# Kernel tuning notes

Hardware: AMD Instinct MI355X
Metric: run time of the kernel (lower is better)

Reference implementation:

```python
import jax, jax.numpy as jnp
import numpy as np

NEG_SLOPE = 0.2


def setup_inputs() -> dict:
    key = jax.random.key(0)
    k1, k2, k3, k4, k5 = jax.random.split(key, 5)
    N, D, E = 10000, 128, 640000
    feat = jax.random.normal(k1, (N, D), dtype=jnp.float32)
    # nn.Linear weight [out_feats, in_feats]; scale like default init
    fc_weight = jax.random.normal(k2, (D, D), dtype=jnp.float32) / jnp.sqrt(jnp.float32(D))
    attn = jax.random.normal(k3, (1, 1, D), dtype=jnp.float32) * 0.1
    eps = jnp.zeros((1,), dtype=jnp.float32)
    src = jax.random.randint(k4, (E,), 0, N, dtype=jnp.int32)
    dst = jax.random.randint(k5, (E,), 0, N, dtype=jnp.int32)
    return {"feat": feat, "fc_weight": fc_weight, "attn": attn, "eps": eps,
            "src": src, "dst": dst}


def reference(feat, fc_weight, attn, eps, src, dst):
    N = feat.shape[0]
    # --- get_attention_tensor (attn_type='MX', num_heads=1) ---
    proj = feat @ fc_weight.T                      # [N, out]
    el = proj[src]                                  # [E, out] u side
    er = proj[dst]                                  # [E, out] v side
    a = attn.reshape(-1)                            # [out]
    e = jnp.sum(jax.nn.leaky_relu(el + er, NEG_SLOPE) * a, axis=-1)   # [E]
    gate = jax.nn.sigmoid(jnp.sum(el * er, axis=-1))                  # [E] sigmoid(u_dot_v)
    w = jax.nn.sigmoid(e * gate)                    # [E] final per-edge weight
    # --- message passing: u_mul_e('h','_edge_weight') with 'mean' reduce ---
    msg = feat[src] * w[:, None]                    # [E, D]
    neigh_sum = jax.ops.segment_sum(msg, dst, num_segments=N)         # [N, D]
    deg = jax.ops.segment_sum(jnp.ones_like(w), dst, num_segments=N)  # [N]
    neigh = neigh_sum / jnp.maximum(deg, 1.0)[:, None]                # mean; 0 for deg-0
    # --- node update ---
    rst = (1.0 + eps[0]) * feat + neigh
    return rst
```

## Files before the change

kernel.cpp:

```cpp
#include <hip/hip_runtime.h>

#define DD 128
#define CAP 128
#define BH 128

typedef unsigned short ushort_t;
typedef __attribute__((ext_vector_type(8))) short bf16x8;
typedef __attribute__((ext_vector_type(4))) float f32x4;

__device__ __forceinline__ unsigned short f2bf(float f) {
    unsigned u = __float_as_uint(f);
    u = (u + 0x7FFFu + ((u >> 16) & 1u)) >> 16;
    return (unsigned short)u;
}
__device__ __forceinline__ float bflo(unsigned v) { return __uint_as_float(v << 16); }
__device__ __forceinline__ float bfhi(unsigned v) { return __uint_as_float(v & 0xFFFF0000u); }
__device__ __forceinline__ unsigned pack2(float a, float b) {
    return (unsigned)f2bf(a) | ((unsigned)f2bf(b) << 16);
}
__device__ __forceinline__ bf16x8 cvt8(const float* __restrict__ p) {
    float4 f0 = *(const float4*)p;
    float4 f1 = *(const float4*)(p + 4);
    bf16x8 v;
    v[0] = (short)f2bf(f0.x); v[1] = (short)f2bf(f0.y);
    v[2] = (short)f2bf(f0.z); v[3] = (short)f2bf(f0.w);
    v[4] = (short)f2bf(f1.x); v[5] = (short)f2bf(f1.y);
    v[6] = (short)f2bf(f1.z); v[7] = (short)f2bf(f1.w);
    return v;
}

__global__ __launch_bounds__(256) void k1_hist_gemm(
    const float* __restrict__ feat, const float* __restrict__ W,
    const float* __restrict__ attn, const int* __restrict__ dst,
    ushort_t* __restrict__ projb, float* __restrict__ dotA,
    ushort_t* __restrict__ cnt, int N, int E, int CE)
{
    extern __shared__ unsigned h[];
    int b = (int)blockIdx.x;
    if (b < BH) {
        int NW = (N + 1) >> 1;
        for (int i = threadIdx.x; i < NW; i += 256) h[i] = 0;
        __syncthreads();
        int base = b * CE;
        for (int k = threadIdx.x; k < CE; k += 256) {
            int i = base + k;
            if (i < E) {
                int d = dst[i];
                atomicAdd(&h[d >> 1], (d & 1) ? 0x10000u : 1u);
            }
        }
        __syncthreads();
        ushort_t* crow = cnt + (size_t)b * N;
        for (int i = threadIdx.x; i < N; i += 256)
            crow[i] = (ushort_t)((h[i >> 1] >> ((i & 1) * 16)) & 0xFFFFu);
        return;
    }
    int rowTile = (b - BH) * 4 + ((int)threadIdx.x >> 6);
    if (rowTile * 16 >= N) return;
    int lane = threadIdx.x & 63;
    int m = lane & 15;
    int quad = lane >> 4;
    const float* arow = feat + (size_t)(rowTile * 16 + m) * DD + quad * 8;
    bf16x8 afr[4];
#pragma unroll
    for (int ks = 0; ks < 4; ++ks) afr[ks] = cvt8(arow + ks * 32);
    float dacc0 = 0.f, dacc1 = 0.f, dacc2 = 0.f, dacc3 = 0.f;
#pragma unroll
    for (int ct = 0; ct < 8; ++ct) {
        const float* brow = W + (size_t)(ct * 16 + m) * DD + quad * 8;
        f32x4 acc = {0.f, 0.f, 0.f, 0.f};
#pragma unroll
        for (int ks = 0; ks < 4; ++ks) {
            bf16x8 bb = cvt8(brow + ks * 32);
            acc = __builtin_amdgcn_mfma_f32_16x16x32_bf16(afr[ks], bb, acc, 0, 0, 0);
        }
        ushort_t* orow = projb + (size_t)(rowTile * 16 + quad * 4) * DD
                       + ct * 16 + m;
#pragma unroll
        for (int r = 0; r < 4; ++r)
            orow[(size_t)r * DD] = f2bf(acc[r]);
        float av = 0.6f * attn[ct * 16 + m];
        dacc0 = fmaf(av, acc[0], dacc0);
        dacc1 = fmaf(av, acc[1], dacc1);
        dacc2 = fmaf(av, acc[2], dacc2);
        dacc3 = fmaf(av, acc[3], dacc3);
    }
#pragma unroll
    for (int o = 1; o < 16; o <<= 1) {
        dacc0 += __shfl_xor(dacc0, o); dacc1 += __shfl_xor(dacc1, o);
        dacc2 += __shfl_xor(dacc2, o); dacc3 += __shfl_xor(dacc3, o);
    }
    if (m == 0) {
        int rbase = rowTile * 16 + quad * 4;
        if (rbase + 3 < N) {
            dotA[rbase]     = dacc0;
            dotA[rbase + 1] = dacc1;
            dotA[rbase + 2] = dacc2;
            dotA[rbase + 3] = dacc3;
        }
    }
}

__global__ __launch_bounds__(256) void k2_scan_cast(
    const float* __restrict__ feat, const ushort_t* __restrict__ cnt,
    ushort_t* __restrict__ offs, int* __restrict__ totals,
    ushort_t* __restrict__ featb, int N, int SC)
{
    int b = (int)blockIdx.x;
    if (b < SC) {
        int bin = b * 256 + (int)threadIdx.x;
        if (bin >= N) return;
        int run = 0;
#pragma unroll 8
        for (int blk = 0; blk < BH; ++blk) {
            int v = cnt[(size_t)blk * N + bin];
            offs[(size_t)blk * N + bin] = (ushort_t)run;
            run += v;
        }
        totals[bin] = run;
        return;
    }
    size_t total = (size_t)N * DD;
    size_t idx = ((size_t)(b - SC) * 256 + threadIdx.x) * 8;
    if (idx + 7 < total) {
        float4 f0 = *(const float4*)(feat + idx);
        float4 f1 = *(const float4*)(feat + idx + 4);
        uint4 o;
        o.x = pack2(f0.x, f0.y); o.y = pack2(f0.z, f0.w);
        o.z = pack2(f1.x, f1.y); o.w = pack2(f1.z, f1.w);
        *(uint4*)(featb + idx) = o;
    } else {
        for (size_t i = idx; i < total; ++i) featb[i] = f2bf(feat[i]);
    }
}

__global__ __launch_bounds__(256) void k3_scatter(
    const int* __restrict__ src, const int* __restrict__ dst,
    const ushort_t* __restrict__ offs, ushort_t* __restrict__ sorted,
    int N, int E, int CE)
{
    extern __shared__ unsigned h[];
    int b = (int)blockIdx.x;
    int NW = (N + 1) >> 1;
    for (int i = threadIdx.x; i < NW; i += 256) h[i] = 0;
    __syncthreads();
    const ushort_t* orow = offs + (size_t)b * N;
    int base = b * CE;
    for (int k = (int)threadIdx.x * 4; k < CE; k += 1024) {
        int i = base + k;
        if (i + 3 < E && k + 3 < CE) {
            int4 s4 = *(const int4*)(src + i);
            int4 d4 = *(const int4*)(dst + i);
            unsigned r0 = atomicAdd(&h[d4.x >> 1], (d4.x & 1) ? 0x10000u : 1u);
            unsigned r1 = atomicAdd(&h[d4.y >> 1], (d4.y & 1) ? 0x10000u : 1u);
            unsigned r2 = atomicAdd(&h[d4.z >> 1], (d4.z & 1) ? 0x10000u : 1u);
            unsigned r3 = atomicAdd(&h[d4.w >> 1], (d4.w & 1) ? 0x10000u : 1u);
            unsigned p0 = (unsigned)orow[d4.x] + ((r0 >> ((d4.x & 1) * 16)) & 0xFFFFu);
            unsigned p1 = (unsigned)orow[d4.y] + ((r1 >> ((d4.y & 1) * 16)) & 0xFFFFu);
            unsigned p2 = (unsigned)orow[d4.z] + ((r2 >> ((d4.z & 1) * 16)) & 0xFFFFu);
            unsigned p3 = (unsigned)orow[d4.w] + ((r3 >> ((d4.w & 1) * 16)) & 0xFFFFu);
            if (p0 < CAP) sorted[(size_t)d4.x * CAP + p0] = (ushort_t)s4.x;
            if (p1 < CAP) sorted[(size_t)d4.y * CAP + p1] = (ushort_t)s4.y;
            if (p2 < CAP) sorted[(size_t)d4.z * CAP + p2] = (ushort_t)s4.z;
            if (p3 < CAP) sorted[(size_t)d4.w * CAP + p3] = (ushort_t)s4.w;
        } else {
            for (int q = 0; q < 4 && k + q < CE; ++q) {
                int ii = base + k + q;
                if (ii < E) {
                    int d = dst[ii];
                    unsigned r = atomicAdd(&h[d >> 1], (d & 1) ? 0x10000u : 1u);
                    unsigned pos = (unsigned)orow[d]
                                 + ((r >> ((d & 1) * 16)) & 0xFFFFu);
                    if (pos < CAP) sorted[(size_t)d * CAP + pos] = (ushort_t)src[ii];
                }
            }
        }
    }
}

__global__ __launch_bounds__(256) void seg_agg(
    const ushort_t* __restrict__ projb, const ushort_t* __restrict__ featb,
    const float* __restrict__ feat, const float* __restrict__ attn,
    const float* __restrict__ dotA, const ushort_t* __restrict__ sorted,
    const int* __restrict__ totals, const float* __restrict__ eps,
    float* __restrict__ out, int N)
{
    int wid = (int)((blockIdx.x * (size_t)blockDim.x + threadIdx.x) >> 6);
    if (wid >= N) return;
    int lane = threadIdx.x & 63;
    int g   = lane >> 3;
    int sub = lane & 7;

    const uint4* projv = (const uint4*)projb;
    const uint4* featv = (const uint4*)featb;

    int m = min(totals[wid], CAP);
    const ushort_t* lst = sorted + (size_t)wid * CAP;

    uint4 ev0 = projv[(size_t)wid * 16 + 2 * sub];
    uint4 ev1 = projv[(size_t)wid * 16 + 2 * sub + 1];
    float er[16] = {
        bflo(ev0.x), bfhi(ev0.x), bflo(ev0.y), bfhi(ev0.y),
        bflo(ev0.z), bfhi(ev0.z), bflo(ev0.w), bfhi(ev0.w),
        bflo(ev1.x), bfhi(ev1.x), bflo(ev1.y), bfhi(ev1.y),
        bflo(ev1.z), bfhi(ev1.z), bflo(ev1.w), bfhi(ev1.w)};
    float av[16];
#pragma unroll
    for (int k = 0; k < 16; ++k) av[k] = 0.4f * attn[16 * sub + k];
    float dAr = dotA[wid];
    float c[16];
#pragma unroll
    for (int k = 0; k < 16; ++k) c[k] = 0.f;

    uint4 apv0, apv1, afv0, afv1; float adAl = 0.f;
    uint4 bpv0, bpv1, bfv0, bfv1; float bdAl = 0.f;

    auto ldst = [&](int idx, uint4& pv0, uint4& pv1, uint4& fv0, uint4& fv1,
                    float& dAl) {
        int s = (idx < m) ? (int)lst[idx] : 0;
        pv0 = projv[(size_t)s * 16 + 2 * sub];
        pv1 = projv[(size_t)s * 16 + 2 * sub + 1];
        fv0 = featv[(size_t)s * 16 + 2 * sub];
        fv1 = featv[(size_t)s * 16 + 2 * sub + 1];
        dAl = dotA[s];
    };

    int i = g;
    if (i < m)     ldst(i,     apv0, apv1, afv0, afv1, adAl);
    if (i + 8 < m) ldst(i + 8, bpv0, bpv1, bfv0, bfv1, bdAl);

    while (i < m) {
        uint4 cpv0, cpv1, cfv0, cfv1; float cdAl;
        ldst(i + 16, cpv0, cpv1, cfv0, cfv1, cdAl);
        float el[16] = {
            bflo(apv0.x), bfhi(apv0.x), bflo(apv0.y), bfhi(apv0.y),
            bflo(apv0.z), bfhi(apv0.z), bflo(apv0.w), bfhi(apv0.w),
            bflo(apv1.x), bfhi(apv1.x), bflo(apv1.y), bfhi(apv1.y),
            bflo(apv1.z), bfhi(apv1.z), bflo(apv1.w), bfhi(apv1.w)};
        float gp = 0.f, ad = 0.f;
#pragma unroll
        for (int k = 0; k < 16; ++k) {
            gp = fmaf(el[k], er[k], gp);
            ad = fmaf(fabsf(el[k] + er[k]), av[k], ad);
        }
#pragma unroll
        for (int o = 1; o <= 4; o <<= 1) {
            gp += __shfl_xor(gp, o);
            ad += __shfl_xor(ad, o);
        }
        float ep = adAl + dAr + ad;
        float gate = 1.f / (1.f + __expf(-gp));
        float w = 1.f / (1.f + __expf(-ep * gate));
        float fl[16] = {
            bflo(afv0.x), bfhi(afv0.x), bflo(afv0.y), bfhi(afv0.y),
            bflo(afv0.z), bfhi(afv0.z), bflo(afv0.w), bfhi(afv0.w),
            bflo(afv1.x), bfhi(afv1.x), bflo(afv1.y), bfhi(afv1.y),
            bflo(afv1.z), bfhi(afv1.z), bflo(afv1.w), bfhi(afv1.w)};
#pragma unroll
        for (int k = 0; k < 16; ++k) c[k] = fmaf(fl[k], w, c[k]);
        apv0 = bpv0; apv1 = bpv1; afv0 = bfv0; afv1 = bfv1; adAl = bdAl;
        bpv0 = cpv0; bpv1 = cpv1; bfv0 = cfv0; bfv1 = cfv1; bdAl = cdAl;
        i += 8;
    }
#pragma unroll
    for (int o = 8; o <= 32; o <<= 1) {
#pragma unroll
        for (int k = 0; k < 16; ++k) c[k] += __shfl_xor(c[k], o);
    }
    if (g == 0) {
        float inv = 1.f / fmaxf((float)m, 1.f);
        float sc = 1.f + eps[0];
        const f32x4* fsrc = (const f32x4*)feat + (size_t)wid * 32 + 4 * sub;
        f32x4* od = (f32x4*)out + (size_t)wid * 32 + 4 * sub;
#pragma unroll
        for (int q = 0; q < 4; ++q) {
            f32x4 f = __builtin_nontemporal_load(&fsrc[q]);
            f32x4 o;
            o[0] = fmaf(sc, f[0], c[4 * q] * inv);
            o[1] = fmaf(sc, f[1], c[4 * q + 1] * inv);
            o[2] = fmaf(sc, f[2], c[4 * q + 2] * inv);
            o[3] = fmaf(sc, f[3], c[4 * q + 3] * inv);
            __builtin_nontemporal_store(o, &od[q]);
        }
    }
}

extern "C" void kernel_launch(void* const* d_in, const int* in_sizes, int n_in,
                              void* d_out, int out_size, void* d_ws, size_t ws_size,
                              hipStream_t stream) {
    const float* feat = (const float*)d_in[0];
    const float* W    = (const float*)d_in[1];
    const float* attn = (const float*)d_in[2];
    const float* eps  = (const float*)d_in[3];
    const int*   src  = (const int*)d_in[4];
    const int*   dst  = (const int*)d_in[5];
    int N = in_sizes[0] / DD;
    int E = in_sizes[4];

    ushort_t* projb  = (ushort_t*)d_ws;
    ushort_t* featb  = projb + (size_t)N * DD;
    ushort_t* sorted = featb + (size_t)N * DD;
    ushort_t* cnt    = sorted + (size_t)N * CAP;
    ushort_t* offs   = cnt + (size_t)BH * N;
    int*      totals = (int*)(offs + (size_t)BH * N);
    float*    dotA   = (float*)(totals + N);

    int CE = (E + BH - 1) / BH;
    int GB = ((N + 15) / 16 + 3) / 4;
    int SC = (N + 255) / 256;
    int CB = (N * DD + 2047) / 2048;
    size_t ldsB = (size_t)((N + 1) / 2) * sizeof(unsigned);

    k1_hist_gemm<<<BH + GB, 256, ldsB, stream>>>(
        feat, W, attn, dst, projb, dotA, cnt, N, E, CE);
    k2_scan_cast<<<SC + CB, 256, 0, stream>>>(
        feat, cnt, offs, totals, featb, N, SC);
    k3_scatter<<<BH, 256, ldsB, stream>>>(src, dst, offs, sorted, N, E, CE);
    seg_agg<<<(N * 64 + 255) / 256, 256, 0, stream>>>(
        projb, featb, feat, attn, dotA, sorted, totals, eps,
        (float*)d_out, N);
}
```

Before: 138.1 us.

## Fuse all four stages into one persistent cooperative kernel with grid syncs

Merges the histogram+GEMM, scan+cast, scatter, and segment aggregation kernels into a single persistent cooperative kernel that loops over virtual blocks and separates the phases with grid.sync(). The aim is to remove the launch overhead and inter-kernel gaps of four launches. In exchange it adds grid-wide barriers and limits parallelism to a capped persistent grid. The per-node aggregation, previously one wave per node, now runs as a grid-stride loop. Each block also carries the 20KB LDS allocation in every phase, which may reduce occupancy.

```diff
diff --git a/kernel.cpp b/kernel.cpp
--- a/kernel.cpp
+++ b/kernel.cpp
@@ -1,4 +1,7 @@
 #include <hip/hip_runtime.h>
+#include <hip/hip_cooperative_groups.h>
+
+namespace cg = cooperative_groups;
 
 #define DD 128
 #define CAP 128
@@ -29,258 +32,249 @@
     return v;
 }
 
-__global__ __launch_bounds__(256) void k1_hist_gemm(
+__global__ __launch_bounds__(256, 4) void fused_all(
     const float* __restrict__ feat, const float* __restrict__ W,
-    const float* __restrict__ attn, const int* __restrict__ dst,
-    ushort_t* __restrict__ projb, float* __restrict__ dotA,
-    ushort_t* __restrict__ cnt, int N, int E, int CE)
+    const float* __restrict__ attn, const int* __restrict__ src,
+    const int* __restrict__ dst, const float* __restrict__ eps,
+    ushort_t* __restrict__ featb, ushort_t* __restrict__ projb,
+    float* __restrict__ dotA, ushort_t* __restrict__ cnt,
+    ushort_t* __restrict__ offs, int* __restrict__ totals,
+    ushort_t* __restrict__ sorted, float* __restrict__ out,
+    int N, int E, int CE, int GB, int CB, int SC)
 {
+    cg::grid_group grid = cg::this_grid();
     extern __shared__ unsigned h[];
-    int b = (int)blockIdx.x;
-    if (b < BH) {
-        int NW = (N + 1) >> 1;
+    int NW = (N + 1) >> 1;
+    int G = (int)gridDim.x;
+
+    for (int vb = (int)blockIdx.x; vb < BH + GB + CB; vb += G) {
+        if (vb < BH) {
+            for (int i = threadIdx.x; i < NW; i += 256) h[i] = 0;
+            __syncthreads();
+            int base = vb * CE;
+            for (int k = threadIdx.x; k < CE; k += 256) {
+                int i = base + k;
+                if (i < E) {
+                    int d = dst[i];
+                    atomicAdd(&h[d >> 1], (d & 1) ? 0x10000u : 1u);
+                }
+            }
+            __syncthreads();
+            ushort_t* crow = cnt + (size_t)vb * N;
+            for (int i = threadIdx.x; i < N; i += 256)
+                crow[i] = (ushort_t)((h[i >> 1] >> ((i & 1) * 16)) & 0xFFFFu);
+            __syncthreads();
+        } else if (vb < BH + GB) {
+            int rowTile = (vb - BH) * 4 + ((int)threadIdx.x >> 6);
+            if (rowTile * 16 < N) {
+                int lane = threadIdx.x & 63;
+                int m = lane & 15;
+                int quad = lane >> 4;
+                const float* arow = feat + (size_t)(rowTile * 16 + m) * DD + quad * 8;
+                bf16x8 afr[4];
+#pragma unroll
+                for (int ks = 0; ks < 4; ++ks) afr[ks] = cvt8(arow + ks * 32);
+                float dacc0 = 0.f, dacc1 = 0.f, dacc2 = 0.f, dacc3 = 0.f;
+#pragma unroll
+                for (int ct = 0; ct < 8; ++ct) {
+                    const float* brow = W + (size_t)(ct * 16 + m) * DD + quad * 8;
+                    f32x4 acc = {0.f, 0.f, 0.f, 0.f};
+#pragma unroll
+                    for (int ks = 0; ks < 4; ++ks) {
+                        bf16x8 bb = cvt8(brow + ks * 32);
+                        acc = __builtin_amdgcn_mfma_f32_16x16x32_bf16(
+                            afr[ks], bb, acc, 0, 0, 0);
+                    }
+                    ushort_t* orow = projb
+                        + (size_t)(rowTile * 16 + quad * 4) * DD + ct * 16 + m;
+#pragma unroll
+                    for (int r = 0; r < 4; ++r)
+                        orow[(size_t)r * DD] = f2bf(acc[r]);
+                    float av = 0.6f * attn[ct * 16 + m];
+                    dacc0 = fmaf(av, acc[0], dacc0);
+                    dacc1 = fmaf(av, acc[1], dacc1);
+                    dacc2 = fmaf(av, acc[2], dacc2);
+                    dacc3 = fmaf(av, acc[3], dacc3);
+                }
+#pragma unroll
+                for (int o = 1; o < 16; o <<= 1) {
+                    dacc0 += __shfl_xor(dacc0, o); dacc1 += __shfl_xor(dacc1, o);
+                    dacc2 += __shfl_xor(dacc2, o); dacc3 += __shfl_xor(dacc3, o);
+                }
+                if (m == 0) {
+                    int rbase = rowTile * 16 + quad * 4;
+                    if (rbase + 3 < N) {
+                        dotA[rbase]     = dacc0;
+                        dotA[rbase + 1] = dacc1;
+                        dotA[rbase + 2] = dacc2;
+                        dotA[rbase + 3] = dacc3;
+                    }
+                }
+            }
+        } else {
+            size_t total = (size_t)N * DD;
+            size_t idx = ((size_t)(vb - BH - GB) * 256 + threadIdx.x) * 8;
+            if (idx + 7 < total) {
+                float4 f0 = *(const float4*)(feat + idx);
+                float4 f1 = *(const float4*)(feat + idx + 4);
+                uint4 o;
+                o.x = pack2(f0.x, f0.y); o.y = pack2(f0.z, f0.w);
+                o.z = pack2(f1.x, f1.y); o.w = pack2(f1.z, f1.w);
+                *(uint4*)(featb + idx) = o;
+            } else {
+                for (size_t i = idx; i < total; ++i) featb[i] = f2bf(feat[i]);
+            }
+        }
+    }
+    grid.sync();
+
+    if ((int)blockIdx.x < SC) {
+        int bin = (int)blockIdx.x * 256 + (int)threadIdx.x;
+        if (bin < N) {
+            int run = 0;
+#pragma unroll 8
+            for (int blk = 0; blk < BH; ++blk) {
+                int v = cnt[(size_t)blk * N + bin];
+                offs[(size_t)blk * N + bin] = (ushort_t)run;
+                run += v;
+            }
+            totals[bin] = run;
+        }
+    }
+    grid.sync();
+
+    for (int vb = (int)blockIdx.x; vb < BH; vb += G) {
         for (int i = threadIdx.x; i < NW; i += 256) h[i] = 0;
         __syncthreads();
-        int base = b * CE;
-        for (int k = threadIdx.x; k < CE; k += 256) {
+        const ushort_t* orow = offs + (size_t)vb * N;
+        int base = vb * CE;
+        for (int k = (int)threadIdx.x * 4; k < CE; k += 1024) {
             int i = base + k;
-            if (i < E) {
-                int d = dst[i];
-                atomicAdd(&h[d >> 1], (d & 1) ? 0x10000u : 1u);
+            if (i + 3 < E && k + 3 < CE) {
+                int4 s4 = *(const int4*)(src + i);
+                int4 d4 = *(const int4*)(dst + i);
+                unsigned r0 = atomicAdd(&h[d4.x >> 1], (d4.x & 1) ? 0x10000u : 1u);
+                unsigned r1 = atomicAdd(&h[d4.y >> 1], (d4.y & 1) ? 0x10000u : 1u);
+                unsigned r2 = atomicAdd(&h[d4.z >> 1], (d4.z & 1) ? 0x10000u : 1u);
+                unsigned r3 = atomicAdd(&h[d4.w >> 1], (d4.w & 1) ? 0x10000u : 1u);
+                unsigned p0 = (unsigned)orow[d4.x] + ((r0 >> ((d4.x & 1) * 16)) & 0xFFFFu);
+                unsigned p1 = (unsigned)orow[d4.y] + ((r1 >> ((d4.y & 1) * 16)) & 0xFFFFu);
+                unsigned p2 = (unsigned)orow[d4.z] + ((r2 >> ((d4.z & 1) * 16)) & 0xFFFFu);
+                unsigned p3 = (unsigned)orow[d4.w] + ((r3 >> ((d4.w & 1) * 16)) & 0xFFFFu);
+                if (p0 < CAP) sorted[(size_t)d4.x * CAP + p0] = (ushort_t)s4.x;
+                if (p1 < CAP) sorted[(size_t)d4.y * CAP + p1] = (ushort_t)s4.y;
+                if (p2 < CAP) sorted[(size_t)d4.z * CAP + p2] = (ushort_t)s4.z;
+                if (p3 < CAP) sorted[(size_t)d4.w * CAP + p3] = (ushort_t)s4.w;
+            } else {
+                for (int q = 0; q < 4 && k + q < CE; ++q) {
+                    int ii = base + k + q;
+                    if (ii < E) {
+                        int d = dst[ii];
+                        unsigned r = atomicAdd(&h[d >> 1], (d & 1) ? 0x10000u : 1u);
+                        unsigned pos = (unsigned)orow[d]
+                                     + ((r >> ((d & 1) * 16)) & 0xFFFFu);
+                        if (pos < CAP) sorted[(size_t)d * CAP + pos] = (ushort_t)src[ii];
+                    }
+                }
             }
         }
         __syncthreads();
-        ushort_t* crow = cnt + (size_t)b * N;
-        for (int i = threadIdx.x; i < N; i += 256)
-            crow[i] = (ushort_t)((h[i >> 1] >> ((i & 1) * 16)) & 0xFFFFu);
-        return;
     }
-    int rowTile = (b - BH) * 4 + ((int)threadIdx.x >> 6);
-    if (rowTile * 16 >= N) return;
-    int lane = threadIdx.x & 63;
-    int m = lane & 15;
-    int quad = lane >> 4;
-    const float* arow = feat + (size_t)(rowTile * 16 + m) * DD + quad * 8;
-    bf16x8 afr[4];
-#pragma unroll
-    for (int ks = 0; ks < 4; ++ks) afr[ks] = cvt8(arow + ks * 32);
-    float dacc0 = 0.f, dacc1 = 0.f, dacc2 = 0.f, dacc3 = 0.f;
-#pragma unroll
-    for (int ct = 0; ct < 8; ++ct) {
-        const float* brow = W + (size_t)(ct * 16 + m) * DD + quad * 8;
-        f32x4 acc = {0.f, 0.f, 0.f, 0.f};
-#pragma unroll
-        for (int ks = 0; ks < 4; ++ks) {
-            bf16x8 bb = cvt8(brow + ks * 32);
-            acc = __builtin_amdgcn_mfma_f32_16x16x32_bf16(afr[ks], bb, acc, 0, 0, 0);
-        }
-        ushort_t* orow = projb + (size_t)(rowTile * 16 + quad * 4) * DD
-                       + ct * 16 + m;
-#pragma unroll
-        for (int r = 0; r < 4; ++r)
-            orow[(size_t)r * DD] = f2bf(acc[r]);
-        float av = 0.6f * attn[ct * 16 + m];
-        dacc0 = fmaf(av, acc[0], dacc0);
-        dacc1 = fmaf(av, acc[1], dacc1);
-        dacc2 = fmaf(av, acc[2], dacc2);
-        dacc3 = fmaf(av, acc[3], dacc3);
-    }
-#pragma unroll
-    for (int o = 1; o < 16; o <<= 1) {
-        dacc0 += __shfl_xor(dacc0, o); dacc1 += __shfl_xor(dacc1, o);
-        dacc2 += __shfl_xor(dacc2, o); dacc3 += __shfl_xor(dacc3, o);
-    }
-    if (m == 0) {
-        int rbase = rowTile * 16 + quad * 4;
-        if (rbase + 3 < N) {
-            dotA[rbase]     = dacc0;
-            dotA[rbase + 1] = dacc1;
-            dotA[rbase + 2] = dacc2;
-            dotA[rbase + 3] = dacc3;
-        }
-    }
-}
-
-__global__ __launch_bounds__(256) void k2_scan_cast(
-    const float* __restrict__ feat, const ushort_t* __restrict__ cnt,
-    ushort_t* __restrict__ offs, int* __restrict__ totals,
-    ushort_t* __restrict__ featb, int N, int SC)
-{
-    int b = (int)blockIdx.x;
-    if (b < SC) {
-        int bin = b * 256 + (int)threadIdx.x;
-        if (bin >= N) return;
-        int run = 0;
-#pragma unroll 8
-        for (int blk = 0; blk < BH; ++blk) {
-            int v = cnt[(size_t)blk * N + bin];
-            offs[(size_t)blk * N + bin] = (ushort_t)run;
-            run += v;
-        }
-        totals[bin] = run;
-        return;
-    }
-    size_t total = (size_t)N * DD;
-    size_t idx = ((size_t)(b - SC) * 256 + threadIdx.x) * 8;
-    if (idx + 7 < total) {
-        float4 f0 = *(const float4*)(feat + idx);
-        float4 f1 = *(const float4*)(feat + idx + 4);
-        uint4 o;
-        o.x = pack2(f0.x, f0.y); o.y = pack2(f0.z, f0.w);
-        o.z = pack2(f1.x, f1.y); o.w = pack2(f1.z, f1.w);
-        *(uint4*)(featb + idx) = o;
-    } else {
-        for (size_t i = idx; i < total; ++i) featb[i] = f2bf(feat[i]);
-    }
-}
-
-__global__ __launch_bounds__(256) void k3_scatter(
-    const int* __restrict__ src, const int* __restrict__ dst,
-    const ushort_t* __restrict__ offs, ushort_t* __restrict__ sorted,
-    int N, int E, int CE)
-{
-    extern __shared__ unsigned h[];
-    int b = (int)blockIdx.x;
-    int NW = (N + 1) >> 1;
-    for (int i = threadIdx.x; i < NW; i += 256) h[i] = 0;
-    __syncthreads();
-    const ushort_t* orow = offs + (size_t)b * N;
-    int base = b * CE;
-    for (int k = (int)threadIdx.x * 4; k < CE; k += 1024) {
-        int i = base + k;
-        if (i + 3 < E && k + 3 < CE) {
-            int4 s4 = *(const int4*)(src + i);
-            int4 d4 = *(const int4*)(dst + i);
-            unsigned r0 = atomicAdd(&h[d4.x >> 1], (d4.x & 1) ? 0x10000u : 1u);
-            unsigned r1 = atomicAdd(&h[d4.y >> 1], (d4.y & 1) ? 0x10000u : 1u);
-            unsigned r2 = atomicAdd(&h[d4.z >> 1], (d4.z & 1) ? 0x10000u : 1u);
-            unsigned r3 = atomicAdd(&h[d4.w >> 1], (d4.w & 1) ? 0x10000u : 1u);
-            unsigned p0 = (unsigned)orow[d4.x] + ((r0 >> ((d4.x & 1) * 16)) & 0xFFFFu);
-            unsigned p1 = (unsigned)orow[d4.y] + ((r1 >> ((d4.y & 1) * 16)) & 0xFFFFu);
-            unsigned p2 = (unsigned)orow[d4.z] + ((r2 >> ((d4.z & 1) * 16)) & 0xFFFFu);
-            unsigned p3 = (unsigned)orow[d4.w] + ((r3 >> ((d4.w & 1) * 16)) & 0xFFFFu);
-            if (p0 < CAP) sorted[(size_t)d4.x * CAP + p0] = (ushort_t)s4.x;
-            if (p1 < CAP) sorted[(size_t)d4.y * CAP + p1] = (ushort_t)s4.y;
-            if (p2 < CAP) sorted[(size_t)d4.z * CAP + p2] = (ushort_t)s4.z;
-            if (p3 < CAP) sorted[(size_t)d4.w * CAP + p3] = (ushort_t)s4.w;
-        } else {
-            for (int q = 0; q < 4 && k + q < CE; ++q) {
-                int ii = base + k + q;
-                if (ii < E) {
-                    int d = dst[ii];
-                    unsigned r = atomicAdd(&h[d >> 1], (d & 1) ? 0x10000u : 1u);
-                    unsigned pos = (unsigned)orow[d]
-                                 + ((r >> ((d & 1) * 16)) & 0xFFFFu);
-                    if (pos < CAP) sorted[(size_t)d * CAP + pos] = (ushort_t)src[ii];
-                }
-            }
-        }
-    }
-}
-
-__global__ __launch_bounds__(256) void seg_agg(
-    const ushort_t* __restrict__ projb, const ushort_t* __restrict__ featb,
-    const float* __restrict__ feat, const float* __restrict__ attn,
-    const float* __restrict__ dotA, const ushort_t* __restrict__ sorted,
-    const int* __restrict__ totals, const float* __restrict__ eps,
-    float* __restrict__ out, int N)
-{
-    int wid = (int)((blockIdx.x * (size_t)blockDim.x + threadIdx.x) >> 6);
-    if (wid >= N) return;
+    grid.sync();
+
     int lane = threadIdx.x & 63;
     int g   = lane >> 3;
     int sub = lane & 7;
-
     const uint4* projv = (const uint4*)projb;
     const uint4* featv = (const uint4*)featb;
-
-    int m = min(totals[wid], CAP);
-    const ushort_t* lst = sorted + (size_t)wid * CAP;
-
-    uint4 ev0 = projv[(size_t)wid * 16 + 2 * sub];
-    uint4 ev1 = projv[(size_t)wid * 16 + 2 * sub + 1];
-    float er[16] = {
-        bflo(ev0.x), bfhi(ev0.x), bflo(ev0.y), bfhi(ev0.y),
-        bflo(ev0.z), bfhi(ev0.z), bflo(ev0.w), bfhi(ev0.w),
-        bflo(ev1.x), bfhi(ev1.x), bflo(ev1.y), bfhi(ev1.y),
-        bflo(ev1.z), bfhi(ev1.z), bflo(ev1.w), bfhi(ev1.w)};
     float av[16];
 #pragma unroll
     for (int k = 0; k < 16; ++k) av[k] = 0.4f * attn[16 * sub + k];
-    float dAr = dotA[wid];
-    float c[16];
-#pragma unroll
-    for (int k = 0; k < 16; ++k) c[k] = 0.f;
-
-    uint4 apv0, apv1, afv0, afv1; float adAl = 0.f;
-    uint4 bpv0, bpv1, bfv0, bfv1; float bdAl = 0.f;
-
-    auto ldst = [&](int idx, uint4& pv0, uint4& pv1, uint4& fv0, uint4& fv1,
-                    float& dAl) {
-        int s = (idx < m) ? (int)lst[idx] : 0;
-        pv0 = projv[(size_t)s * 16 + 2 * sub];
-        pv1 = projv[(size_t)s * 16 + 2 * sub + 1];
-        fv0 = featv[(size_t)s * 16 + 2 * sub];
-        fv1 = featv[(size_t)s * 16 + 2 * sub + 1];
-        dAl = dotA[s];
-    };
-
-    int i = g;
-    if (i < m)     ldst(i,     apv0, apv1, afv0, afv1, adAl);
-    if (i + 8 < m) ldst(i + 8, bpv0, bpv1, bfv0, bfv1, bdAl);
-
-    while (i < m) {
-        uint4 cpv0, cpv1, cfv0, cfv1; float cdAl;
-        ldst(i + 16, cpv0, cpv1, cfv0, cfv1, cdAl);
-        float el[16] = {
-            bflo(apv0.x), bfhi(apv0.x), bflo(apv0.y), bfhi(apv0.y),
-            bflo(apv0.z), bfhi(apv0.z), bflo(apv0.w), bfhi(apv0.w),
-            bflo(apv1.x), bfhi(apv1.x), bflo(apv1.y), bfhi(apv1.y),
-            bflo(apv1.z), bfhi(apv1.z), bflo(apv1.w), bfhi(apv1.w)};
-        float gp = 0.f, ad = 0.f;
-#pragma unroll
-        for (int k = 0; k < 16; ++k) {
-            gp = fmaf(el[k], er[k], gp);
-            ad = fmaf(fabsf(el[k] + er[k]), av[k], ad);
-        }
-#pragma unroll
-        for (int o = 1; o <= 4; o <<= 1) {
-            gp += __shfl_xor(gp, o);
-            ad += __shfl_xor(ad, o);
-        }
-        float ep = adAl + dAr + ad;
-        float gate = 1.f / (1.f + __expf(-gp));
-        float w = 1.f / (1.f + __expf(-ep * gate));
-        float fl[16] = {
-            bflo(afv0.x), bfhi(afv0.x), bflo(afv0.y), bfhi(afv0.y),
-            bflo(afv0.z), bfhi(afv0.z), bflo(afv0.w), bfhi(afv0.w),
-            bflo(afv1.x), bfhi(afv1.x), bflo(afv1.y), bfhi(afv1.y),
-            bflo(afv1.z), bfhi(afv1.z), bflo(afv1.w), bfhi(afv1.w)};
-#pragma unroll
-        for (int k = 0; k < 16; ++k) c[k] = fmaf(fl[k], w, c[k]);
-        apv0 = bpv0; apv1 = bpv1; afv0 = bfv0; afv1 = bfv1; adAl = bdAl;
-        bpv0 = cpv0; bpv1 = cpv1; bfv0 = cfv0; bfv1 = cfv1; bdAl = cdAl;
-        i += 8;
-    }
-#pragma unroll
-    for (int o = 8; o <= 32; o <<= 1) {
-#pragma unroll
-        for (int k = 0; k < 16; ++k) c[k] += __shfl_xor(c[k], o);
-    }
-    if (g == 0) {
-        float inv = 1.f / fmaxf((float)m, 1.f);
-        float sc = 1.f + eps[0];
-        const f32x4* fsrc = (const f32x4*)feat + (size_t)wid * 32 + 4 * sub;
-        f32x4* od = (f32x4*)out + (size_t)wid * 32 + 4 * sub;
-#pragma unroll
-        for (int q = 0; q < 4; ++q) {
-            f32x4 f = __builtin_nontemporal_load(&fsrc[q]);
-            f32x4 o;
-            o[0] = fmaf(sc, f[0], c[4 * q] * inv);
-            o[1] = fmaf(sc, f[1], c[4 * q + 1] * inv);
-            o[2] = fmaf(sc, f[2], c[4 * q + 2] * inv);
-            o[3] = fmaf(sc, f[3], c[4 * q + 3] * inv);
-            __builtin_nontemporal_store(o, &od[q]);
+    float sc = 1.f + eps[0];
+    int totalWaves = G * 4;
+    int gw = (int)blockIdx.x * 4 + ((int)threadIdx.x >> 6);
+
+    for (int wid = gw; wid < N; wid += totalWaves) {
+        int m = min(totals[wid], CAP);
+        const ushort_t* lst = sorted + (size_t)wid * CAP;
+        uint4 ev0 = projv[(size_t)wid * 16 + 2 * sub];
+        uint4 ev1 = projv[(size_t)wid * 16 + 2 * sub + 1];
+        float er[16] = {
+            bflo(ev0.x), bfhi(ev0.x), bflo(ev0.y), bfhi(ev0.y),
+            bflo(ev0.z), bfhi(ev0.z), bflo(ev0.w), bfhi(ev0.w),
+            bflo(ev1.x), bfhi(ev1.x), bflo(ev1.y), bfhi(ev1.y),
+            bflo(ev1.z), bfhi(ev1.z), bflo(ev1.w), bfhi(ev1.w)};
+        float dAr = dotA[wid];
+        float c[16];
+#pragma unroll
+        for (int k = 0; k < 16; ++k) c[k] = 0.f;
+
+        uint4 apv0, apv1, afv0, afv1; float adAl = 0.f;
+        uint4 bpv0, bpv1, bfv0, bfv1; float bdAl = 0.f;
+        auto ldst = [&](int idx, uint4& pv0, uint4& pv1, uint4& fv0,
+                        uint4& fv1, float& dAl) {
+            int s = (idx < m) ? (int)lst[idx] : 0;
+            pv0 = projv[(size_t)s * 16 + 2 * sub];
+            pv1 = projv[(size_t)s * 16 + 2 * sub + 1];
+            fv0 = featv[(size_t)s * 16 + 2 * sub];
+            fv1 = featv[(size_t)s * 16 + 2 * sub + 1];
+            dAl = dotA[s];
+        };
+        int i = g;
+        if (i < m)     ldst(i,     apv0, apv1, afv0, afv1, adAl);
+        if (i + 8 < m) ldst(i + 8, bpv0, bpv1, bfv0, bfv1, bdAl);
+        while (i < m) {
+            uint4 cpv0, cpv1, cfv0, cfv1; float cdAl;
+            ldst(i + 16, cpv0, cpv1, cfv0, cfv1, cdAl);
+            float el[16] = {
+                bflo(apv0.x), bfhi(apv0.x), bflo(apv0.y), bfhi(apv0.y),
+                bflo(apv0.z), bfhi(apv0.z), bflo(apv0.w), bfhi(apv0.w),
+                bflo(apv1.x), bfhi(apv1.x), bflo(apv1.y), bfhi(apv1.y),
+                bflo(apv1.z), bfhi(apv1.z), bflo(apv1.w), bfhi(apv1.w)};
+            float gp = 0.f, ad = 0.f;
+#pragma unroll
+            for (int k = 0; k < 16; ++k) {
+                gp = fmaf(el[k], er[k], gp);
+                ad = fmaf(fabsf(el[k] + er[k]), av[k], ad);
+            }
+#pragma unroll
+            for (int o = 1; o <= 4; o <<= 1) {
+                gp += __shfl_xor(gp, o);
+                ad += __shfl_xor(ad, o);
+            }
+            float ep = adAl + dAr + ad;
+            float gate = 1.f / (1.f + __expf(-gp));
+            float w = 1.f / (1.f + __expf(-ep * gate));
+            float fl[16] = {
+                bflo(afv0.x), bfhi(afv0.x), bflo(afv0.y), bfhi(afv0.y),
+                bflo(afv0.z), bfhi(afv0.z), bflo(afv0.w), bfhi(afv0.w),
+                bflo(afv1.x), bfhi(afv1.x), bflo(afv1.y), bfhi(afv1.y),
+                bflo(afv1.z), bfhi(afv1.z), bflo(afv1.w), bfhi(afv1.w)};
+#pragma unroll
+            for (int k = 0; k < 16; ++k) c[k] = fmaf(fl[k], w, c[k]);
+            apv0 = bpv0; apv1 = bpv1; afv0 = bfv0; afv1 = bfv1; adAl = bdAl;
+            bpv0 = cpv0; bpv1 = cpv1; bfv0 = cfv0; bfv1 = cfv1; bdAl = cdAl;
+            i += 8;
+        }
+#pragma unroll
+        for (int o = 8; o <= 32; o <<= 1) {
+#pragma unroll
+            for (int k = 0; k < 16; ++k) c[k] += __shfl_xor(c[k], o);
+        }
+        if (g == 0) {
+            float inv = 1.f / fmaxf((float)m, 1.f);
+            const f32x4* fsrc = (const f32x4*)feat + (size_t)wid * 32 + 4 * sub;
+            f32x4* od = (f32x4*)out + (size_t)wid * 32 + 4 * sub;
+#pragma unroll
+            for (int q = 0; q < 4; ++q) {
+                f32x4 f = __builtin_nontemporal_load(&fsrc[q]);
+                f32x4 o;
+                o[0] = fmaf(sc, f[0], c[4 * q] * inv);
+                o[1] = fmaf(sc, f[1], c[4 * q + 1] * inv);
+                o[2] = fmaf(sc, f[2], c[4 * q + 2] * inv);
+                o[3] = fmaf(sc, f[3], c[4 * q + 3] * inv);
+                __builtin_nontemporal_store(o, &od[q]);
+            }
         }
     }
 }
@@ -304,19 +298,27 @@
     ushort_t* offs   = cnt + (size_t)BH * N;
     int*      totals = (int*)(offs + (size_t)BH * N);
     float*    dotA   = (float*)(totals + N);
+    float*    out    = (float*)d_out;
 
     int CE = (E + BH - 1) / BH;
     int GB = ((N + 15) / 16 + 3) / 4;
+    int CB = (N * DD + 2047) / 2048;
     int SC = (N + 255) / 256;
-    int CB = (N * DD + 2047) / 2048;
     size_t ldsB = (size_t)((N + 1) / 2) * sizeof(unsigned);
 
-    k1_hist_gemm<<<BH + GB, 256, ldsB, stream>>>(
-        feat, W, attn, dst, projb, dotA, cnt, N, E, CE);
-    k2_scan_cast<<<SC + CB, 256, 0, stream>>>(
-        feat, cnt, offs, totals, featb, N, SC);
-    k3_scatter<<<BH, 256, ldsB, stream>>>(src, dst, offs, sorted, N, E, CE);
-    seg_agg<<<(N * 64 + 255) / 256, 256, 0, stream>>>(
-        projb, featb, feat, attn, dotA, sorted, totals, eps,
-        (float*)d_out, N);
-}
+    int maxBlocksPerCU = 0;
+    hipOccupancyMaxActiveBlocksPerMultiprocessor(
+        &maxBlocksPerCU, (const void*)fused_all, 256, ldsB);
+    int G = maxBlocksPerCU * 256;
+    if (G > 1024) G = 1024;
+    if (G < 256) G = 256;
+
+    void* args[] = {
+        (void*)&feat, (void*)&W, (void*)&attn, (void*)&src, (void*)&dst,
+        (void*)&eps, (void*)&featb, (void*)&projb, (void*)&dotA,
+        (void*)&cnt, (void*)&offs, (void*)&totals, (void*)&sorted,
+        (void*)&out, (void*)&N, (void*)&E, (void*)&CE, (void*)&GB,
+        (void*)&CB, (void*)&SC};
+    hipLaunchCooperativeKernel((const void*)fused_all, dim3(G), dim3(256),
+                               args, (unsigned)ldsB, stream);
+}
```

After: 337.6 us. 145% more time.

## Merge cast into GEMM kernel and fuse scan with scatter via flag

Applied to the files above, without the earlier changes.

Moves the feature-to-bf16 cast into the histogram/GEMM launch, and merges the per-bin prefix scan with the scatter kernel. Scatter blocks spin on a global atomic counter until every scan block has released its offsets. This removes one kernel launch and its inter-kernel gap. It relies on the scan blocks being scheduled before or alongside the spinning scatter blocks; with SC+BH blocks this should fit on the device, but the spin-wait can stall or deadlock if residency assumptions fail.

```diff
diff --git a/kernel.cpp b/kernel.cpp
--- a/kernel.cpp
+++ b/kernel.cpp
@@ -29,14 +29,16 @@
     return v;
 }
 
-__global__ __launch_bounds__(256) void k1_hist_gemm(
+__global__ __launch_bounds__(256) void k1_hist_gemm_cast(
     const float* __restrict__ feat, const float* __restrict__ W,
     const float* __restrict__ attn, const int* __restrict__ dst,
-    ushort_t* __restrict__ projb, float* __restrict__ dotA,
-    ushort_t* __restrict__ cnt, int N, int E, int CE)
+    ushort_t* __restrict__ featb, ushort_t* __restrict__ projb,
+    float* __restrict__ dotA, ushort_t* __restrict__ cnt,
+    int* __restrict__ flag, int N, int E, int GB, int CE)
 {
     extern __shared__ unsigned h[];
     int b = (int)blockIdx.x;
+    if (b == BH && threadIdx.x == 0) *flag = 0;
     if (b < BH) {
         int NW = (N + 1) >> 1;
         for (int i = threadIdx.x; i < NW; i += 256) h[i] = 0;
@@ -55,73 +57,55 @@
             crow[i] = (ushort_t)((h[i >> 1] >> ((i & 1) * 16)) & 0xFFFFu);
         return;
     }
-    int rowTile = (b - BH) * 4 + ((int)threadIdx.x >> 6);
-    if (rowTile * 16 >= N) return;
-    int lane = threadIdx.x & 63;
-    int m = lane & 15;
-    int quad = lane >> 4;
-    const float* arow = feat + (size_t)(rowTile * 16 + m) * DD + quad * 8;
-    bf16x8 afr[4];
-#pragma unroll
-    for (int ks = 0; ks < 4; ++ks) afr[ks] = cvt8(arow + ks * 32);
-    float dacc0 = 0.f, dacc1 = 0.f, dacc2 = 0.f, dacc3 = 0.f;
-#pragma unroll
-    for (int ct = 0; ct < 8; ++ct) {
-        const float* brow = W + (size_t)(ct * 16 + m) * DD + quad * 8;
-        f32x4 acc = {0.f, 0.f, 0.f, 0.f};
-#pragma unroll
-        for (int ks = 0; ks < 4; ++ks) {
-            bf16x8 bb = cvt8(brow + ks * 32);
-            acc = __builtin_amdgcn_mfma_f32_16x16x32_bf16(afr[ks], bb, acc, 0, 0, 0);
-        }
-        ushort_t* orow = projb + (size_t)(rowTile * 16 + quad * 4) * DD
-                       + ct * 16 + m;
-#pragma unroll
-        for (int r = 0; r < 4; ++r)
-            orow[(size_t)r * DD] = f2bf(acc[r]);
-        float av = 0.6f * attn[ct * 16 + m];
-        dacc0 = fmaf(av, acc[0], dacc0);
-        dacc1 = fmaf(av, acc[1], dacc1);
-        dacc2 = fmaf(av, acc[2], dacc2);
-        dacc3 = fmaf(av, acc[3], dacc3);
-    }
-#pragma unroll
-    for (int o = 1; o < 16; o <<= 1) {
-        dacc0 += __shfl_xor(dacc0, o); dacc1 += __shfl_xor(dacc1, o);
-        dacc2 += __shfl_xor(dacc2, o); dacc3 += __shfl_xor(dacc3, o);
-    }
-    if (m == 0) {
-        int rbase = rowTile * 16 + quad * 4;
-        if (rbase + 3 < N) {
-            dotA[rbase]     = dacc0;
-            dotA[rbase + 1] = dacc1;
-            dotA[rbase + 2] = dacc2;
-            dotA[rbase + 3] = dacc3;
-        }
-    }
-}
-
-__global__ __launch_bounds__(256) void k2_scan_cast(
-    const float* __restrict__ feat, const ushort_t* __restrict__ cnt,
-    ushort_t* __restrict__ offs, int* __restrict__ totals,
-    ushort_t* __restrict__ featb, int N, int SC)
-{
-    int b = (int)blockIdx.x;
-    if (b < SC) {
-        int bin = b * 256 + (int)threadIdx.x;
-        if (bin >= N) return;
-        int run = 0;
-#pragma unroll 8
-        for (int blk = 0; blk < BH; ++blk) {
-            int v = cnt[(size_t)blk * N + bin];
-            offs[(size_t)blk * N + bin] = (ushort_t)run;
-            run += v;
-        }
-        totals[bin] = run;
+    if (b < BH + GB) {
+        int rowTile = (b - BH) * 4 + ((int)threadIdx.x >> 6);
+        if (rowTile * 16 >= N) return;
+        int lane = threadIdx.x & 63;
+        int m = lane & 15;
+        int quad = lane >> 4;
+        const float* arow = feat + (size_t)(rowTile * 16 + m) * DD + quad * 8;
+        bf16x8 afr[4];
+#pragma unroll
+        for (int ks = 0; ks < 4; ++ks) afr[ks] = cvt8(arow + ks * 32);
+        float dacc0 = 0.f, dacc1 = 0.f, dacc2 = 0.f, dacc3 = 0.f;
+#pragma unroll
+        for (int ct = 0; ct < 8; ++ct) {
+            const float* brow = W + (size_t)(ct * 16 + m) * DD + quad * 8;
+            f32x4 acc = {0.f, 0.f, 0.f, 0.f};
+#pragma unroll
+            for (int ks = 0; ks < 4; ++ks) {
+                bf16x8 bb = cvt8(brow + ks * 32);
+                acc = __builtin_amdgcn_mfma_f32_16x16x32_bf16(afr[ks], bb, acc, 0, 0, 0);
+            }
+            ushort_t* orow = projb + (size_t)(rowTile * 16 + quad * 4) * DD
+                           + ct * 16 + m;
+#pragma unroll
+            for (int r = 0; r < 4; ++r)
+                orow[(size_t)r * DD] = f2bf(acc[r]);
+            float av = 0.6f * attn[ct * 16 + m];
+            dacc0 = fmaf(av, acc[0], dacc0);
+            dacc1 = fmaf(av, acc[1], dacc1);
+            dacc2 = fmaf(av, acc[2], dacc2);
+            dacc3 = fmaf(av, acc[3], dacc3);
+        }
+#pragma unroll
+        for (int o = 1; o < 16; o <<= 1) {
+            dacc0 += __shfl_xor(dacc0, o); dacc1 += __shfl_xor(dacc1, o);
+            dacc2 += __shfl_xor(dacc2, o); dacc3 += __shfl_xor(dacc3, o);
+        }
+        if (m == 0) {
+            int rbase = rowTile * 16 + quad * 4;
+            if (rbase + 3 < N) {
+                dotA[rbase]     = dacc0;
+                dotA[rbase + 1] = dacc1;
+                dotA[rbase + 2] = dacc2;
+                dotA[rbase + 3] = dacc3;
+            }
+        }
         return;
     }
     size_t total = (size_t)N * DD;
-    size_t idx = ((size_t)(b - SC) * 256 + threadIdx.x) * 8;
+    size_t idx = ((size_t)(b - BH - GB) * 256 + threadIdx.x) * 8;
     if (idx + 7 < total) {
         float4 f0 = *(const float4*)(feat + idx);
         float4 f1 = *(const float4*)(feat + idx + 4);
@@ -134,18 +118,46 @@
     }
 }
 
-__global__ __launch_bounds__(256) void k3_scatter(
+__global__ __launch_bounds__(256) void k23_scan_scatter(
     const int* __restrict__ src, const int* __restrict__ dst,
-    const ushort_t* __restrict__ offs, ushort_t* __restrict__ sorted,
-    int N, int E, int CE)
+    const ushort_t* __restrict__ cnt, ushort_t* __restrict__ offs,
+    int* __restrict__ totals, ushort_t* __restrict__ sorted,
+    int* __restrict__ flag, int N, int E, int CE, int SC)
 {
     extern __shared__ unsigned h[];
     int b = (int)blockIdx.x;
+    if (b < SC) {
+        int bin = b * 256 + (int)threadIdx.x;
+        if (bin < N) {
+            int run = 0;
+#pragma unroll 8
+            for (int blk = 0; blk < BH; ++blk) {
+                int v = cnt[(size_t)blk * N + bin];
+                offs[(size_t)blk * N + bin] = (ushort_t)run;
+                run += v;
+            }
+            totals[bin] = run;
+        }
+        __threadfence();
+        __syncthreads();
+        if (threadIdx.x == 0)
+            __hip_atomic_fetch_add(flag, 1, __ATOMIC_RELEASE,
+                                   __HIP_MEMORY_SCOPE_AGENT);
+        return;
+    }
+    int vb = b - SC;
     int NW = (N + 1) >> 1;
     for (int i = threadIdx.x; i < NW; i += 256) h[i] = 0;
     __syncthreads();
-    const ushort_t* orow = offs + (size_t)b * N;
-    int base = b * CE;
+    if (threadIdx.x == 0) {
+        while (__hip_atomic_load(flag, __ATOMIC_ACQUIRE,
+                                 __HIP_MEMORY_SCOPE_AGENT) < SC)
+            __builtin_amdgcn_s_sleep(2);
+        __threadfence();
+    }
+    __syncthreads();
+    const ushort_t* orow = offs + (size_t)vb * N;
+    int base = vb * CE;
     for (int k = (int)threadIdx.x * 4; k < CE; k += 1024) {
         int i = base + k;
         if (i + 3 < E && k + 3 < CE) {
@@ -304,18 +316,18 @@
     ushort_t* offs   = cnt + (size_t)BH * N;
     int*      totals = (int*)(offs + (size_t)BH * N);
     float*    dotA   = (float*)(totals + N);
+    int*      flag   = (int*)(dotA + N);
 
     int CE = (E + BH - 1) / BH;
     int GB = ((N + 15) / 16 + 3) / 4;
+    int CB = (N * DD + 2047) / 2048;
     int SC = (N + 255) / 256;
-    int CB = (N * DD + 2047) / 2048;
     size_t ldsB = (size_t)((N + 1) / 2) * sizeof(unsigned);
 
-    k1_hist_gemm<<<BH + GB, 256, ldsB, stream>>>(
-        feat, W, attn, dst, projb, dotA, cnt, N, E, CE);
-    k2_scan_cast<<<SC + CB, 256, 0, stream>>>(
-        feat, cnt, offs, totals, featb, N, SC);
-    k3_scatter<<<BH, 256, ldsB, stream>>>(src, dst, offs, sorted, N, E, CE);
+    k1_hist_gemm_cast<<<BH + GB + CB, 256, ldsB, stream>>>(
+        feat, W, attn, dst, featb, projb, dotA, cnt, flag, N, E, GB, CE);
+    k23_scan_scatter<<<SC + BH, 256, ldsB, stream>>>(
+        src, dst, cnt, offs, totals, sorted, flag, N, E, CE, SC);
     seg_agg<<<(N * 64 + 255) / 256, 256, 0, stream>>>(
         projb, featb, feat, attn, dotA, sorted, totals, eps,
         (float*)d_out, N);
```

After: 161.2 us. +16.7%, slower.
